# Kernel tuning notes

Measured on AMD Instinct MI355X. Metric: run time of the kernel, lower is better.

The kernel has to match this reference:

```python
import jax, jax.numpy as jnp
import numpy as np

B, C, HS, WS = 4, 256, 64, 64
NK, NV, NH = 32, 32, 8
QKV = NK * NV + NK + NV  # 1088


def setup_inputs() -> dict:
    key = jax.random.key(0)
    k1, k2, k3, k4 = jax.random.split(key, 4)
    x = jax.random.normal(k1, (B, C, HS, WS), dtype=jnp.float32)
    Wqkv = jax.random.normal(k2, (NH, QKV, C), dtype=jnp.float32) * (C ** -0.5)
    Wc = jax.random.normal(k3, (C, NV * NH), dtype=jnp.float32) * ((NV * NH) ** -0.5)
    bc = jax.random.normal(k4, (C,), dtype=jnp.float32) * 0.01
    return {"x": x, "Wqkv": Wqkv, "Wc": Wc, "bc": bc}


def reference(x, Wqkv, Wc, bc):
    b, c, h, w = x.shape
    n = h * w
    xt = x.reshape(b, c, n).transpose(0, 2, 1)  # (B, N, C)
    # All heads' QKV projections in one einsum (torch loops over heads)
    qkv = jnp.einsum('bnc,hqc->bhnq', xt, Wqkv)  # (B, NH, N, QKV)
    q = qkv[..., :NK]                                            # (B,NH,N,NK)
    k = qkv[..., NK:NK + NK * NV].reshape(b, NH, n, NK, NV)      # (B,NH,N,NK,NV)
    v = qkv[..., NK + NK * NV:]                                  # (B,NH,N,NV)
    # per-pixel tiny matmul: (1xNK) @ (NKxNV) -> NV, scaled
    qk = jnp.einsum('bhnk,bhnkv->bhnv', q, k) / (NK ** 0.5)
    a = jax.nn.softmax(qk, axis=-1) * v  # (B, NH, N, NV)
    # concat heads along channel dim (head-major), then combine Linear
    a = a.transpose(0, 2, 1, 3).reshape(b, n, NH * NV)  # (B, N, NH*NV)
    out = a @ Wc.T + bc  # (B, N, C)
    return out.transpose(0, 2, 1).reshape(b, c, h, w)
```

## Files before the change

kernel.cpp:

```cpp
#include <hip/hip_runtime.h>

#define NPIX_TOTAL 16384
#define CDIM 256
#define NHEADS 8
#define QKVD 1088
#define NQKV 8704

typedef unsigned short u16;
typedef __attribute__((ext_vector_type(8))) __bf16 bf16x8;
typedef __attribute__((ext_vector_type(4))) float f32x4;
typedef __attribute__((ext_vector_type(2))) unsigned u32x2;

__device__ static inline u16 f2bf(float f) {
  union { float f; unsigned u; } x; x.f = f;
  unsigned r = x.u + 0x7fffu + ((x.u >> 16) & 1u);
  return (u16)(r >> 16);
}

__device__ static inline void gload_lds16(const void* g, void* l) {
  __builtin_amdgcn_global_load_lds((const __attribute__((address_space(1))) void*)g,
                                   (__attribute__((address_space(3))) void*)l,
                                   16, 0, 0);
}

#define WAITVM(N) asm volatile("s_waitcnt vmcnt(" #N ")" ::: "memory")
#define BARRIER() asm volatile("s_barrier" ::: "memory")

__global__ __launch_bounds__(256) void transpose_cast(const float* __restrict__ x,
                                                      u16* __restrict__ xt) {
  __shared__ float t[64][65];
  const int b = blockIdx.z;
  const float* xb = x + (size_t)b * CDIM * 4096;
  u16* ob = xt + (size_t)b * 4096 * CDIM;
  const int n0 = blockIdx.x * 64;
  const int c0 = blockIdx.y * 64;
  const int tx = threadIdx.x & 63;
  const int ty = threadIdx.x >> 6;
#pragma unroll
  for (int i = 0; i < 16; ++i)
    t[ty + i * 4][tx] = xb[(size_t)(c0 + ty + i * 4) * 4096 + n0 + tx];
  __syncthreads();
#pragma unroll
  for (int i = 0; i < 16; ++i)
    ob[(size_t)(n0 + ty + i * 4) * CDIM + c0 + tx] = f2bf(t[tx][ty + i * 4]);
}

__global__ __launch_bounds__(256) void cast_bf(const float* __restrict__ in,
                                               u16* __restrict__ out, int n) {
  const int i = (blockIdx.x * 256 + threadIdx.x) * 4;
  if (i >= n) return;
  const f32x4 v = *(const f32x4*)(in + i);
  *(unsigned*)(out + i) = (unsigned)f2bf(v.x) | ((unsigned)f2bf(v.y) << 16);
  *(unsigned*)(out + i + 2) = (unsigned)f2bf(v.z) | ((unsigned)f2bf(v.w) << 16);
}

__global__ __launch_bounds__(512, 2) void fused_qkv_attn(const u16* __restrict__ Xbf,
                                                         const u16* __restrict__ Wbf,
                                                         u16* __restrict__ Abf) {
  __shared__ u16 A_lds[128 * 256];
  __shared__ u16 Bring[4][128 * 64];
  __shared__ float q_lds[128 * 32];

  const int tid = threadIdx.x;
  const int lane = tid & 63;
  const int l15 = lane & 15;
  const int hi = lane >> 4;
  const int wid = tid >> 6;
  const int wr = wid >> 2;
  const int wn = wid & 3;
  const int wm = wr * 64;

  const int head = blockIdx.x & 7;
  const int pixtile = blockIdx.x >> 3;
  const u16* Ag = Xbf + (size_t)pixtile * 128 * CDIM;
  const u16* Wh = Wbf + (size_t)head * QKVD * CDIM;

#pragma unroll
  for (int i = 0; i < 8; ++i) {
    const int seg = wid * 8 + i;
    const int L = seg * 64 + lane;
    const int row = L >> 5;
    const int c = L & 31;
    const int cs = (c & 24) | ((c & 7) ^ (row & 7));
    gload_lds16(Ag + (size_t)row * CDIM + cs * 8, (char*)A_lds + (size_t)seg * 1024);
  }
#pragma unroll
  for (int i = 0; i < 4; ++i) {
    const int seg = wid * 4 + i;
    const int L = seg * 64 + lane;
    const int row = L >> 5;
    const int c = L & 31;
    const int cs = (c & 24) | ((c & 7) ^ (row & 7));
    const int grow = row < 32 ? row : row + 1024;
    gload_lds16(Wh + (size_t)grow * CDIM + cs * 8, (char*)&Bring[0][0] + (size_t)seg * 1024);
  }
  WAITVM(0);
  __syncthreads();

  auto afrag = [&](int mi, int kb, int kk2) -> bf16x8 {
    const int row = wm + mi * 16 + l15;
    const int ch = kb * 8 + ((kk2 * 4 + hi) ^ (row & 7));
    return *(const bf16x8*)(A_lds + row * 256 + ch * 8);
  };

  f32x4 accq[4] = {};
  const int brow = wn * 16 + l15;
#pragma unroll
  for (int kb = 0; kb < 4; ++kb)
#pragma unroll
    for (int kk2 = 0; kk2 < 2; ++kk2) {
      const int bch = kb * 8 + ((kk2 * 4 + hi) ^ (brow & 7));
      const bf16x8 bq = *(const bf16x8*)(&Bring[0][0] + brow * 256 + bch * 8);
#pragma unroll
      for (int mi = 0; mi < 4; ++mi)
        accq[mi] = __builtin_amdgcn_mfma_f32_16x16x32_bf16(bq, afrag(mi, kb, kk2),
                                                           accq[mi], 0, 0, 0);
    }
  if (wn < 2) {
#pragma unroll
    for (int mi = 0; mi < 4; ++mi) {
      const int pix = wm + mi * 16 + l15;
      *(f32x4*)(q_lds + pix * 32 + ((wn * 4 + hi) ^ (pix & 7)) * 4) = accq[mi];
    }
  }
  __syncthreads();

  f32x4 acc[4][2] = {};
  f32x4 qkr[4][2] = {};
  bf16x8 afc[4][2];

  auto stage = [&](int t) {
    const int kb = t >> 3, sh = t & 7;
    u16* dst = &Bring[t & 3][0];
#pragma unroll
    for (int i = 0; i < 2; ++i) {
      const int L = i * 512 + wid * 64 + lane;
      const int row = L >> 3;
      const int c8 = (L & 7) ^ (row & 7);
      gload_lds16(Wh + (size_t)(32 + sh * 128 + row) * CDIM + kb * 64 + c8 * 8,
                  (char*)dst + (size_t)(i * 512 + wid * 64) * 16);
    }
  };

  auto step = [&](int t) {
    const int sh = t & 7;
    if (sh == 0) {
      const int kb = t >> 3;
#pragma unroll
      for (int mi = 0; mi < 4; ++mi)
#pragma unroll
        for (int kk2 = 0; kk2 < 2; ++kk2) afc[mi][kk2] = afrag(mi, kb, kk2);
    }
    const u16* bs = &Bring[t & 3][0];
    bf16x8 bfr[2][2];
#pragma unroll
    for (int ni = 0; ni < 2; ++ni)
#pragma unroll
      for (int kk2 = 0; kk2 < 2; ++kk2) {
        const int rr = wn * 32 + ni * 16 + l15;
        bfr[ni][kk2] = *(const bf16x8*)(bs + rr * 64 + (((kk2 * 4 + hi) ^ (rr & 7))) * 8);
      }
    __builtin_amdgcn_s_setprio(1);
#pragma unroll
    for (int mi = 0; mi < 4; ++mi)
#pragma unroll
      for (int ni = 0; ni < 2; ++ni)
#pragma unroll
        for (int kk2 = 0; kk2 < 2; ++kk2)
          acc[mi][ni] = __builtin_amdgcn_mfma_f32_16x16x32_bf16(bfr[ni][kk2], afc[mi][kk2],
                                                                acc[mi][ni], 0, 0, 0);
    __builtin_amdgcn_s_setprio(0);
#pragma unroll
    for (int mi = 0; mi < 4; ++mi) {
      const int pix = wm + mi * 16 + l15;
      const float qv_ = q_lds[pix * 32 + (sh ^ (pix & 7)) * 4 + wn];
      qkr[mi][0] += qv_ * acc[mi][0];
      qkr[mi][1] += qv_ * acc[mi][1];
      acc[mi][0] = (f32x4){0.f, 0.f, 0.f, 0.f};
      acc[mi][1] = (f32x4){0.f, 0.f, 0.f, 0.f};
    }
  };

  stage(0); stage(1); stage(2);
#pragma unroll 1
  for (int t = 0; t < 30; ++t) {
    WAITVM(4);
    BARRIER();
    if (t < 29) stage(t + 3);
    step(t);
  }
  WAITVM(2); BARRIER(); step(30);
  WAITVM(0); BARRIER(); step(31);

  __syncthreads();
  float* part = (float*)A_lds;
#pragma unroll
  for (int mi = 0; mi < 4; ++mi)
#pragma unroll
    for (int par = 0; par < 2; ++par) {
      const int pix = wm + mi * 16 + l15;
      const int ch = (par * 4 + hi) ^ (pix & 7);
      *(f32x4*)(part + wn * 4096 + pix * 32 + ch * 4) = qkr[mi][par];
    }
  __syncthreads();

  const float scale = 0.17677669529663687f;
#pragma unroll
  for (int mi = 0; mi < 4; ++mi) {
    const int pix = wm + mi * 16 + l15;
    const int ch0 = hi ^ (pix & 7);
    const int ch1 = (4 + hi) ^ (pix & 7);
    f32x4 q0 = {0.f, 0.f, 0.f, 0.f}, q1 = {0.f, 0.f, 0.f, 0.f};
#pragma unroll
    for (int w = 0; w < 4; ++w) {
      q0 += *(const f32x4*)(part + w * 4096 + pix * 32 + ch0 * 4);
      q1 += *(const f32x4*)(part + w * 4096 + pix * 32 + ch1 * 4);
    }
    q0 *= scale; q1 *= scale;
    float m = fmaxf(fmaxf(fmaxf(q0.x, q0.y), fmaxf(q0.z, q0.w)),
                    fmaxf(fmaxf(q1.x, q1.y), fmaxf(q1.z, q1.w)));
    m = fmaxf(m, __shfl_xor(m, 16));
    m = fmaxf(m, __shfl_xor(m, 32));
    f32x4 e0, e1;
    e0.x = __expf(q0.x - m); e0.y = __expf(q0.y - m);
    e0.z = __expf(q0.z - m); e0.w = __expf(q0.w - m);
    e1.x = __expf(q1.x - m); e1.y = __expf(q1.y - m);
    e1.z = __expf(q1.z - m); e1.w = __expf(q1.w - m);
    float su = e0.x + e0.y + e0.z + e0.w + e1.x + e1.y + e1.z + e1.w;
    su += __shfl_xor(su, 16);
    su += __shfl_xor(su, 32);
    if (wn >= 2) {
      const float inv = 1.0f / su;
      const f32x4 a = (wn == 2 ? e0 : e1) * (accq[mi] * inv);
      u32x2 p;
      p.x = (unsigned)f2bf(a.x) | ((unsigned)f2bf(a.y) << 16);
      p.y = (unsigned)f2bf(a.z) | ((unsigned)f2bf(a.w) << 16);
      const size_t gp = (size_t)(pixtile * 128 + pix) * 256 + head * 32 + (wn - 2) * 16 + hi * 4;
      *(u32x2*)(Abf + gp) = p;
    }
  }
}

__global__ __launch_bounds__(256, 2) void gemm_out(const u16* __restrict__ A,
                                                   const u16* __restrict__ B,
                                                   float* __restrict__ Cout,
                                                   const float* __restrict__ bias) {
  __shared__ u16 As[2][128 * 64];
  __shared__ u16 Bs[2][128 * 64];
  const int tid = threadIdx.x;
  const int lane = tid & 63;
  const int wv = tid >> 6;
  const size_t m0 = (size_t)blockIdx.y * 128;
  const size_t n0 = (size_t)blockIdx.x * 128;
  const int wm = (wv >> 1) * 64;
  const int wn = (wv & 1) * 64;
  const int frow = lane & 15;
  const int fh = lane >> 4;
  const int fsw = frow & 7;

  f32x4 acc[4][4] = {};

  auto stage = [&](int buf, int kt) {
#pragma unroll
    for (int i = 0; i < 4; ++i) {
      const int L = (i * 4 + wv) * 64 + lane;
      const int r = L >> 3;
      const int cs = (L & 7) ^ (r & 7);
      const size_t goff = (size_t)r * CDIM + kt * 64 + cs * 8;
      gload_lds16(A + m0 * CDIM + goff, (char*)As[buf] + (size_t)(i * 4 + wv) * 1024);
      gload_lds16(B + n0 * CDIM + goff, (char*)Bs[buf] + (size_t)(i * 4 + wv) * 1024);
    }
  };

  stage(0, 0);
#pragma unroll
  for (int kt = 0; kt < 4; ++kt) {
    __syncthreads();
    if (kt < 3) stage((kt + 1) & 1, kt + 1);
    const u16* as = As[kt & 1];
    const u16* bs = Bs[kt & 1];
#pragma unroll
    for (int kk2 = 0; kk2 < 2; ++kk2) {
      const int kc = (kk2 * 4 + fh) ^ fsw;
      bf16x8 af[4], bfr[4];
#pragma unroll
      for (int mi = 0; mi < 4; ++mi)
        af[mi] = *(const bf16x8*)(as + (wm + mi * 16 + frow) * 64 + kc * 8);
#pragma unroll
      for (int ni = 0; ni < 4; ++ni)
        bfr[ni] = *(const bf16x8*)(bs + (wn + ni * 16 + frow) * 64 + kc * 8);
#pragma unroll
      for (int mi = 0; mi < 4; ++mi)
#pragma unroll
        for (int ni = 0; ni < 4; ++ni)
          acc[mi][ni] =
              __builtin_amdgcn_mfma_f32_16x16x32_bf16(af[mi], bfr[ni], acc[mi][ni], 0, 0, 0);
    }
  }

#pragma unroll
  for (int mi = 0; mi < 4; ++mi)
#pragma unroll
    for (int ni = 0; ni < 4; ++ni) {
      const size_t gm = m0 + wm + mi * 16 + fh * 4;
      const size_t gn = n0 + wn + ni * 16 + frow;
      f32x4 v = acc[mi][ni];
      v += bias[gn];
      const size_t b = gm >> 12;
      const size_t pix = gm & 4095;
      *(f32x4*)(Cout + ((b << 8) + gn) * 4096 + pix) = v;
    }
}

extern "C" void kernel_launch(void* const* d_in, const int* in_sizes, int n_in,
                              void* d_out, int out_size, void* d_ws, size_t ws_size,
                              hipStream_t stream) {
  (void)in_sizes; (void)n_in; (void)out_size; (void)ws_size;
  const float* x = (const float*)d_in[0];
  const float* Wqkv = (const float*)d_in[1];
  const float* Wc = (const float*)d_in[2];
  const float* bc = (const float*)d_in[3];
  float* out = (float*)d_out;
  char* ws = (char*)d_ws;

  const size_t XBF_OFF = 0;
  const size_t WBF_OFF = 8388608;
  const size_t WCBF_OFF = 12845056;
  const size_t ABF_OFF = 12976128;
  u16* Xbf = (u16*)(ws + XBF_OFF);
  u16* Wbf = (u16*)(ws + WBF_OFF);
  u16* Wcbf = (u16*)(ws + WCBF_OFF);
  u16* Abf = (u16*)(ws + ABF_OFF);

  transpose_cast<<<dim3(64, 4, 4), 256, 0, stream>>>(x, Xbf);
  cast_bf<<<(NQKV * CDIM) / 1024, 256, 0, stream>>>(Wqkv, Wbf, NQKV * CDIM);
  cast_bf<<<(CDIM * 256) / 1024, 256, 0, stream>>>(Wc, Wcbf, CDIM * 256);

  fused_qkv_attn<<<dim3((NPIX_TOTAL / 128) * NHEADS), 512, 0, stream>>>(Xbf, Wbf, Abf);

  gemm_out<<<dim3(256 / 128, NPIX_TOTAL / 128), 256, 0, stream>>>(Abf, Wcbf, out, bc);
}
```

Baseline: 135.0 us.

## Halve pixel tile in fused QKV-attention kernel to 64 pixels with 4 waves

Shrinks each fused_qkv_attn block from 128 pixels and 8 waves to 64 pixels and 4 waves. The K-weight stream is restaged in 64-row slices over 64 pipeline steps, and each wave now owns one 16-column slice, so the cross-wave partial reduction shrinks from 4 to 2 terms. This doubles the grid and halves LDS per block, which should raise occupancy and wave parallelism. In exchange every block re-streams the full per-head K weights for half as many pixels, doubling weight traffic through L2.

```diff
diff --git a/kernel.cpp b/kernel.cpp
--- a/kernel.cpp
+++ b/kernel.cpp
@@ -54,30 +54,28 @@
   *(unsigned*)(out + i + 2) = (unsigned)f2bf(v.z) | ((unsigned)f2bf(v.w) << 16);
 }
 
-__global__ __launch_bounds__(512, 2) void fused_qkv_attn(const u16* __restrict__ Xbf,
+__global__ __launch_bounds__(256, 2) void fused_qkv_attn(const u16* __restrict__ Xbf,
                                                          const u16* __restrict__ Wbf,
                                                          u16* __restrict__ Abf) {
-  __shared__ u16 A_lds[128 * 256];
-  __shared__ u16 Bring[4][128 * 64];
-  __shared__ float q_lds[128 * 32];
+  __shared__ u16 A_lds[64 * 256];
+  __shared__ u16 Bring[4][64 * 64];
+  __shared__ float q_lds[64 * 32];
 
   const int tid = threadIdx.x;
   const int lane = tid & 63;
   const int l15 = lane & 15;
   const int hi = lane >> 4;
-  const int wid = tid >> 6;
-  const int wr = wid >> 2;
-  const int wn = wid & 3;
-  const int wm = wr * 64;
+  const int wn = tid >> 6;
 
   const int head = blockIdx.x & 7;
   const int pixtile = blockIdx.x >> 3;
-  const u16* Ag = Xbf + (size_t)pixtile * 128 * CDIM;
+  const u16* Ag = Xbf + (size_t)pixtile * 64 * CDIM;
   const u16* Wh = Wbf + (size_t)head * QKVD * CDIM;
+  u16* ring = &Bring[0][0];
 
 #pragma unroll
   for (int i = 0; i < 8; ++i) {
-    const int seg = wid * 8 + i;
+    const int seg = wn * 8 + i;
     const int L = seg * 64 + lane;
     const int row = L >> 5;
     const int c = L & 31;
@@ -85,20 +83,20 @@
     gload_lds16(Ag + (size_t)row * CDIM + cs * 8, (char*)A_lds + (size_t)seg * 1024);
   }
 #pragma unroll
-  for (int i = 0; i < 4; ++i) {
-    const int seg = wid * 4 + i;
+  for (int i = 0; i < 8; ++i) {
+    const int seg = wn * 8 + i;
     const int L = seg * 64 + lane;
     const int row = L >> 5;
     const int c = L & 31;
     const int cs = (c & 24) | ((c & 7) ^ (row & 7));
     const int grow = row < 32 ? row : row + 1024;
-    gload_lds16(Wh + (size_t)grow * CDIM + cs * 8, (char*)&Bring[0][0] + (size_t)seg * 1024);
+    gload_lds16(Wh + (size_t)grow * CDIM + cs * 8, (char*)ring + (size_t)seg * 1024);
   }
   WAITVM(0);
   __syncthreads();
 
   auto afrag = [&](int mi, int kb, int kk2) -> bf16x8 {
-    const int row = wm + mi * 16 + l15;
+    const int row = mi * 16 + l15;
     const int ch = kb * 8 + ((kk2 * 4 + hi) ^ (row & 7));
     return *(const bf16x8*)(A_lds + row * 256 + ch * 8);
   };
@@ -110,7 +108,7 @@
 #pragma unroll
     for (int kk2 = 0; kk2 < 2; ++kk2) {
       const int bch = kb * 8 + ((kk2 * 4 + hi) ^ (brow & 7));
-      const bf16x8 bq = *(const bf16x8*)(&Bring[0][0] + brow * 256 + bch * 8);
+      const bf16x8 bq = *(const bf16x8*)(ring + brow * 256 + bch * 8);
 #pragma unroll
       for (int mi = 0; mi < 4; ++mi)
         accq[mi] = __builtin_amdgcn_mfma_f32_16x16x32_bf16(bq, afrag(mi, kb, kk2),
@@ -119,103 +117,90 @@
   if (wn < 2) {
 #pragma unroll
     for (int mi = 0; mi < 4; ++mi) {
-      const int pix = wm + mi * 16 + l15;
+      const int pix = mi * 16 + l15;
       *(f32x4*)(q_lds + pix * 32 + ((wn * 4 + hi) ^ (pix & 7)) * 4) = accq[mi];
     }
   }
   __syncthreads();
 
-  f32x4 acc[4][2] = {};
-  f32x4 qkr[4][2] = {};
+  f32x4 qkr[4] = {};
   bf16x8 afc[4][2];
 
   auto stage = [&](int t) {
-    const int kb = t >> 3, sh = t & 7;
+    const int kb = t >> 4, s = t & 15;
     u16* dst = &Bring[t & 3][0];
 #pragma unroll
     for (int i = 0; i < 2; ++i) {
-      const int L = i * 512 + wid * 64 + lane;
+      const int L = (wn * 2 + i) * 64 + lane;
       const int row = L >> 3;
       const int c8 = (L & 7) ^ (row & 7);
-      gload_lds16(Wh + (size_t)(32 + sh * 128 + row) * CDIM + kb * 64 + c8 * 8,
-                  (char*)dst + (size_t)(i * 512 + wid * 64) * 16);
+      gload_lds16(Wh + (size_t)(32 + s * 64 + row) * CDIM + kb * 64 + c8 * 8,
+                  (char*)dst + (size_t)(wn * 2 + i) * 1024);
     }
   };
 
   auto step = [&](int t) {
-    const int sh = t & 7;
-    if (sh == 0) {
-      const int kb = t >> 3;
+    const int s = t & 15;
+    if (s == 0) {
+      const int kb = t >> 4;
 #pragma unroll
       for (int mi = 0; mi < 4; ++mi)
 #pragma unroll
         for (int kk2 = 0; kk2 < 2; ++kk2) afc[mi][kk2] = afrag(mi, kb, kk2);
     }
     const u16* bs = &Bring[t & 3][0];
-    bf16x8 bfr[2][2];
-#pragma unroll
-    for (int ni = 0; ni < 2; ++ni)
-#pragma unroll
-      for (int kk2 = 0; kk2 < 2; ++kk2) {
-        const int rr = wn * 32 + ni * 16 + l15;
-        bfr[ni][kk2] = *(const bf16x8*)(bs + rr * 64 + (((kk2 * 4 + hi) ^ (rr & 7))) * 8);
-      }
+    const int rr = wn * 16 + l15;
+    bf16x8 bfr0 = *(const bf16x8*)(bs + rr * 64 + ((hi ^ (rr & 7))) * 8);
+    bf16x8 bfr1 = *(const bf16x8*)(bs + rr * 64 + (((4 + hi) ^ (rr & 7))) * 8);
+    f32x4 acc[4];
     __builtin_amdgcn_s_setprio(1);
 #pragma unroll
-    for (int mi = 0; mi < 4; ++mi)
-#pragma unroll
-      for (int ni = 0; ni < 2; ++ni)
-#pragma unroll
-        for (int kk2 = 0; kk2 < 2; ++kk2)
-          acc[mi][ni] = __builtin_amdgcn_mfma_f32_16x16x32_bf16(bfr[ni][kk2], afc[mi][kk2],
-                                                                acc[mi][ni], 0, 0, 0);
+    for (int mi = 0; mi < 4; ++mi) {
+      acc[mi] = __builtin_amdgcn_mfma_f32_16x16x32_bf16(bfr0, afc[mi][0],
+                                                        (f32x4){0.f, 0.f, 0.f, 0.f}, 0, 0, 0);
+      acc[mi] = __builtin_amdgcn_mfma_f32_16x16x32_bf16(bfr1, afc[mi][1], acc[mi], 0, 0, 0);
+    }
     __builtin_amdgcn_s_setprio(0);
+    const int k = s * 2 + (wn >> 1);
 #pragma unroll
     for (int mi = 0; mi < 4; ++mi) {
-      const int pix = wm + mi * 16 + l15;
-      const float qv_ = q_lds[pix * 32 + (sh ^ (pix & 7)) * 4 + wn];
-      qkr[mi][0] += qv_ * acc[mi][0];
-      qkr[mi][1] += qv_ * acc[mi][1];
-      acc[mi][0] = (f32x4){0.f, 0.f, 0.f, 0.f};
-      acc[mi][1] = (f32x4){0.f, 0.f, 0.f, 0.f};
+      const int pix = mi * 16 + l15;
+      const float qv_ = q_lds[pix * 32 + ((k >> 2) ^ (pix & 7)) * 4 + (k & 3)];
+      qkr[mi] += qv_ * acc[mi];
     }
   };
 
   stage(0); stage(1); stage(2);
 #pragma unroll 1
-  for (int t = 0; t < 30; ++t) {
+  for (int t = 0; t < 61; ++t) {
     WAITVM(4);
     BARRIER();
-    if (t < 29) stage(t + 3);
+    stage(t + 3);
     step(t);
   }
-  WAITVM(2); BARRIER(); step(30);
-  WAITVM(0); BARRIER(); step(31);
+  WAITVM(4); BARRIER(); step(61);
+  WAITVM(2); BARRIER(); step(62);
+  WAITVM(0); BARRIER(); step(63);
 
   __syncthreads();
   float* part = (float*)A_lds;
 #pragma unroll
-  for (int mi = 0; mi < 4; ++mi)
-#pragma unroll
-    for (int par = 0; par < 2; ++par) {
-      const int pix = wm + mi * 16 + l15;
-      const int ch = (par * 4 + hi) ^ (pix & 7);
-      *(f32x4*)(part + wn * 4096 + pix * 32 + ch * 4) = qkr[mi][par];
-    }
+  for (int mi = 0; mi < 4; ++mi) {
+    const int pix = mi * 16 + l15;
+    const int chs = hi ^ (pix & 3) ^ ((pix >> 2) & 3);
+    *(f32x4*)(part + wn * 1024 + pix * 16 + chs * 4) = qkr[mi];
+  }
   __syncthreads();
 
   const float scale = 0.17677669529663687f;
 #pragma unroll
   for (int mi = 0; mi < 4; ++mi) {
-    const int pix = wm + mi * 16 + l15;
-    const int ch0 = hi ^ (pix & 7);
-    const int ch1 = (4 + hi) ^ (pix & 7);
-    f32x4 q0 = {0.f, 0.f, 0.f, 0.f}, q1 = {0.f, 0.f, 0.f, 0.f};
-#pragma unroll
-    for (int w = 0; w < 4; ++w) {
-      q0 += *(const f32x4*)(part + w * 4096 + pix * 32 + ch0 * 4);
-      q1 += *(const f32x4*)(part + w * 4096 + pix * 32 + ch1 * 4);
-    }
+    const int pix = mi * 16 + l15;
+    const int ch = (hi ^ (pix & 3) ^ ((pix >> 2) & 3)) * 4;
+    f32x4 q0 = *(const f32x4*)(part + 0 * 1024 + pix * 16 + ch) +
+               *(const f32x4*)(part + 2 * 1024 + pix * 16 + ch);
+    f32x4 q1 = *(const f32x4*)(part + 1 * 1024 + pix * 16 + ch) +
+               *(const f32x4*)(part + 3 * 1024 + pix * 16 + ch);
     q0 *= scale; q1 *= scale;
     float m = fmaxf(fmaxf(fmaxf(q0.x, q0.y), fmaxf(q0.z, q0.w)),
                     fmaxf(fmaxf(q1.x, q1.y), fmaxf(q1.z, q1.w)));
@@ -235,7 +220,7 @@
       u32x2 p;
       p.x = (unsigned)f2bf(a.x) | ((unsigned)f2bf(a.y) << 16);
       p.y = (unsigned)f2bf(a.z) | ((unsigned)f2bf(a.w) << 16);
-      const size_t gp = (size_t)(pixtile * 128 + pix) * 256 + head * 32 + (wn - 2) * 16 + hi * 4;
+      const size_t gp = (size_t)(pixtile * 64 + pix) * 256 + head * 32 + (wn - 2) * 16 + hi * 4;
       *(u32x2*)(Abf + gp) = p;
     }
   }
@@ -336,7 +321,7 @@
   cast_bf<<<(NQKV * CDIM) / 1024, 256, 0, stream>>>(Wqkv, Wbf, NQKV * CDIM);
   cast_bf<<<(CDIM * 256) / 1024, 256, 0, stream>>>(Wc, Wcbf, CDIM * 256);
 
-  fused_qkv_attn<<<dim3((NPIX_TOTAL / 128) * NHEADS), 512, 0, stream>>>(Xbf, Wbf, Abf);
+  fused_qkv_attn<<<dim3((NPIX_TOTAL / 64) * NHEADS), 256, 0, stream>>>(Xbf, Wbf, Abf);
 
   gemm_out<<<dim3(256 / 128, NPIX_TOTAL / 128), 256, 0, stream>>>(Abf, Wcbf, out, bc);
 }
```

Result: slower. 148.3 us (+9.9%).
